# Performance work log

Hardware: AMD Instinct MI355X
Metric: run time of the kernel (lower is better)

The kernel has to match this reference:

```python
import jax, jax.numpy as jnp
import numpy as np

B, T, K, V = 64, 256, 32, 32  # batch, trace_len, net_k, vocab_len


def setup_inputs() -> dict:
    key = jax.random.key(0)
    k1, k2, k3 = jax.random.split(key, 3)
    x = jax.random.uniform(k1, (B, T, V), dtype=jnp.float32)
    w_right = jax.random.normal(k2, (K, K + 1), dtype=jnp.float32)
    w_op = jax.random.normal(k3, (K, 5 + V), dtype=jnp.float32)
    return {"x": x, "w_right": w_right, "w_op": w_op}


def _myrelu(z):
    # CenteredLayer: x<0 -> 0.01*x ; x>1 -> 0.01*x + 0.99 ; else identity
    return jnp.where(z < 0, 0.01 * z, jnp.where(z > 1, 0.01 * z + 0.99, z))


def reference(x, w_right, w_op):
    Bs, Ts, Vs = x.shape
    Ks = w_right.shape[0]
    # cal_softmax()
    sm_op = jax.nn.softmax(w_op, axis=1)
    op_w = sm_op[:, :5].T          # (5, K) operator selection weights
    atom_w = sm_op[:, 5:].T        # (V, K)
    right_w = jax.nn.softmax(w_right, axis=1)[:, :-1].T  # (K, K)

    # atom_x is loop-invariant (x and atom_w do not change across iterations)
    atom_x = jnp.einsum('btv,vk->btk', x, atom_w)  # (B, T, K)
    zcol = jnp.zeros((Bs, Ts, 1), x.dtype)   # last_x (always zeros)
    zrow = jnp.zeros((Bs, 1, Ks), x.dtype)   # end_x  (always zeros)

    def step(all_x, _):
        left = jnp.concatenate([all_x[:, :, 1:], zcol], axis=2)          # shift node dim
        right = jnp.einsum('btk,kj->btj', all_x, right_w)                # right-child mix
        nxt = all_x[:, 1:]                                               # (B, T-1, K)
        X_left = jnp.concatenate(
            [jnp.concatenate([nxt[:, :, 1:], zcol[:, 1:]], axis=2), zrow], axis=1)
        nxt_full = jnp.concatenate([nxt, zrow], axis=1)                  # (B, T, K)
        until = right + _myrelu(left + nxt_full - 1.0)
        new = _myrelu(atom_x
                      + (1.0 - left) * op_w[1]            # not
                      + X_left * op_w[3]                  # next (X)
                      + (left + right - 1.0) * op_w[2]    # and
                      + until * op_w[4])                  # until
        return new, None

    init = jnp.zeros((Bs, Ts, Ks), x.dtype)
    all_x, _ = jax.lax.scan(step, init, None, length=Ts + Ks)
    return jax.nn.sigmoid((all_x - 0.5) * 5.0)
```

## Files before the change

kernel.cpp:

```cpp
#include <hip/hip_runtime.h>
#include <math.h>

#define BB 64
#define TT 256
#define KK 32
#define VV 32
#define CH 32
#define PH 32
#define ROWS (CH + PH)
#define NPHASE ((TT + KK) / PH)
#define BPB (TT / CH)
#define NW (ROWS / 16)

#define RW_OFF    0
#define WOP_OFF   1024
#define ATOM_OFF  2240
#define STATE_OFF (ATOM_OFF + BB*TT*KK)
#define FLAG_OFF  (STATE_OFF + BB*TT*KK)

typedef __attribute__((ext_vector_type(8))) short short8;
typedef __attribute__((ext_vector_type(4))) float floatx4;

__device__ __forceinline__ float myrelu(float z) {
    return fmaf(0.01f, z, 0.99f * __builtin_amdgcn_fmed3f(z, 0.f, 1.f));
}
__device__ __forceinline__ ushort f2bf(float f) {
    union { float f; unsigned int u; } v; v.f = f;
    unsigned int r = v.u + 0x7fffu + ((v.u >> 16) & 1u);
    return (ushort)(r >> 16);
}
__device__ __forceinline__ float dpp_shl1(float v) {
    return __int_as_float(__builtin_amdgcn_update_dpp(
        0, __float_as_int(v), 0x101 , 0xF, 0xF, true));
}

__global__ void prep_kernel(const float* __restrict__ w_right,
                            const float* __restrict__ w_op,
                            float* __restrict__ ws) {
    int tid = threadIdx.x;
    float* rw  = ws + RW_OFF;
    float* wop = ws + WOP_OFF;
    if (tid < KK) {
        float v[37];
        float m = -1e30f;
        #pragma unroll
        for (int i = 0; i < 37; ++i) { v[i] = w_op[tid * 37 + i]; m = fmaxf(m, v[i]); }
        float s = 0.f;
        #pragma unroll
        for (int i = 0; i < 37; ++i) { v[i] = expf(v[i] - m); s += v[i]; }
        float inv = 1.f / s;
        #pragma unroll
        for (int i = 0; i < 37; ++i) wop[i * KK + tid] = v[i] * inv;
    } else if (tid < 2 * KK) {
        int r = tid - KK;
        float v[KK + 1];
        float m = -1e30f;
        #pragma unroll
        for (int i = 0; i <= KK; ++i) { v[i] = w_right[r * (KK + 1) + i]; m = fmaxf(m, v[i]); }
        float s = 0.f;
        #pragma unroll
        for (int i = 0; i <= KK; ++i) { v[i] = expf(v[i] - m); s += v[i]; }
        float inv = 1.f / s;
        #pragma unroll
        for (int c = 0; c < KK; ++c) rw[c * KK + r] = v[c] * inv;
    }
}

__global__ void atomx_kernel(const float* __restrict__ x, float* __restrict__ ws) {
    const float* aw = ws + WOP_OFF + 5 * KK;
    float* atom = ws + ATOM_OFF;
    int tid = threadIdx.x;
    if (blockIdx.x < 2) ((int*)(ws + FLAG_OFF))[blockIdx.x * 256 + tid] = 0;
    int k  = tid & (KK - 1);
    int bt = blockIdx.x * 8 + (tid >> 5);
    const float* xrow = x + bt * VV;
    float acc = 0.f;
    #pragma unroll
    for (int v = 0; v < VV; ++v) acc = fmaf(xrow[v], aw[v * KK + k], acc);
    atom[bt * KK + k] = acc;
}

__global__ __launch_bounds__(256, 2)
void phase_all_kernel(float* __restrict__ ws, float* __restrict__ out) {
    __shared__ float brow[2][NW + 1][36];

    const float* rw   = ws + RW_OFF;
    const float* wop  = ws + WOP_OFF;
    const float* atom = ws + ATOM_OFF;
    float*      state = ws + STATE_OFF;
    int*        flags = (int*)(ws + FLAG_OFF);

    int tid  = threadIdx.x;
    int lane = tid & 63;
    int rt   = tid >> 6;
    int lr   = lane & 15;
    int hi   = lane >> 4;
    int b  = blockIdx.x / BPB;
    int c  = blockIdx.x % BPB;
    int lo = c * CH;
    int t0 = lo + rt * 16 + lr;
    bool active = (lo + rt * 16) < TT;

    for (int i = tid; i < 2 * (NW + 1) * 36; i += 256)
        (&brow[0][0][0])[i] = 0.f;

    float* gs = state + (size_t)b * TT * KK;

    float y[8];
    #pragma unroll
    for (int q = 0; q < 8; ++q) y[q] = 0.f;

    float c0p[8], d1p[8], w3v[8], w4n[8], w4c[8];
    {
        float av[8] = {0, 0, 0, 0, 0, 0, 0, 0};
        if (active) {
            float4 a0 = *reinterpret_cast<const float4*>(&atom[((size_t)b * TT + t0) * KK + hi * 8]);
            float4 a1 = *reinterpret_cast<const float4*>(&atom[((size_t)b * TT + t0) * KK + hi * 8 + 4]);
            av[0] = a0.x; av[1] = a0.y; av[2] = a0.z; av[3] = a0.w;
            av[4] = a1.x; av[5] = a1.y; av[6] = a1.z; av[7] = a1.w;
        }
        #pragma unroll
        for (int q = 0; q < 8; ++q) {
            int j = hi * 8 + q;
            float w1 = wop[1 * KK + j];
            float w2 = wop[2 * KK + j];
            float w3 = wop[3 * KK + j];
            float w4 = wop[4 * KK + j];
            c0p[q] = av[q] + w1 - w2 - w4;
            d1p[q] = (w2 - w1) + 0.01f * w4;
            w4n[q] = 0.01f * w4;
            w4c[q] = 0.99f * w4;
            w3v[q] = w3;
        }
    }

    short8 af0, af1;
    {
        int col0 = ((lr >> 2) << 3) | (lr & 3);
        float s0 = wop[2 * KK + col0]     + wop[4 * KK + col0];
        float s1 = wop[2 * KK + col0 + 4] + wop[4 * KK + col0 + 4];
        #pragma unroll
        for (int q = 0; q < 8; ++q) {
            af0[q] = (short)f2bf(rw[(hi * 8 + q) * KK + col0] * s0);
            af1[q] = (short)f2bf(rw[(hi * 8 + q) * KK + col0 + 4] * s1);
        }
    }

    int pidx = ((lane + 16) & 63) << 2;
    __syncthreads();

    for (int p = 0; p < NPHASE; ++p) {
        for (int s = 0; s < PH; ++s) {
            int cur = s & 1;
            if (active) {
                unsigned bw0, bw1, bw2, bw3;
                asm("v_cvt_pk_bf16_f32 %0, %1, %2" : "=v"(bw0) : "v"(y[0]), "v"(y[1]));
                asm("v_cvt_pk_bf16_f32 %0, %1, %2" : "=v"(bw1) : "v"(y[2]), "v"(y[3]));
                asm("v_cvt_pk_bf16_f32 %0, %1, %2" : "=v"(bw2) : "v"(y[4]), "v"(y[5]));
                asm("v_cvt_pk_bf16_f32 %0, %1, %2" : "=v"(bw3) : "v"(y[6]), "v"(y[7]));
                union { unsigned u[4]; short8 v; } bu;
                bu.u[0] = bw0; bu.u[1] = bw1; bu.u[2] = bw2; bu.u[3] = bw3;
                floatx4 acc0 = __builtin_amdgcn_mfma_f32_16x16x32_bf16(
                    af0, bu.v, (floatx4){c0p[0], c0p[1], c0p[2], c0p[3]}, 0, 0, 0);
                floatx4 acc1 = __builtin_amdgcn_mfma_f32_16x16x32_bf16(
                    af1, bu.v, (floatx4){c0p[4], c0p[5], c0p[6], c0p[7]}, 0, 0, 0);

                float nx[8];
                #pragma unroll
                for (int q = 0; q < 8; ++q) nx[q] = dpp_shl1(y[q]);
                float lbr = __int_as_float(__builtin_amdgcn_ds_bpermute(pidx, __float_as_int(y[0])));
                float lb  = (hi == 3) ? 0.f : lbr;
                float xb  = dpp_shl1(lb);
                if (hi == 3) xb = 0.f;
                if (lr == 15) {
                    float4 n0 = *reinterpret_cast<const float4*>(&brow[cur][rt + 1][hi * 8]);
                    float4 n1 = *reinterpret_cast<const float4*>(&brow[cur][rt + 1][hi * 8 + 4]);
                    nx[0] = n0.x; nx[1] = n0.y; nx[2] = n0.z; nx[3] = n0.w;
                    nx[4] = n1.x; nx[5] = n1.y; nx[6] = n1.z; nx[7] = n1.w;
                    xb = brow[cur][rt + 1][hi * 8 + 8];
                }

                float le[8], xl[8];
                #pragma unroll
                for (int q = 0; q < 7; ++q) { le[q] = y[q + 1]; xl[q] = nx[q + 1]; }
                le[7] = lb; xl[7] = xb;

                #pragma unroll
                for (int q = 0; q < 8; ++q) {
                    float accq = (q < 4) ? acc0[q] : acc1[q - 4];
                    float sm = le[q] + nx[q];
                    float t  = __builtin_amdgcn_fmed3f(sm, 1.f, 2.f);
                    float z  = fmaf(le[q], d1p[q],
                               fmaf(nx[q], w4n[q],
                               fmaf(t, w4c[q],
                               fmaf(xl[q], w3v[q], accq))));
                    y[q] = myrelu(z);
                }
                if (lr == 0) {
                    *reinterpret_cast<float4*>(&brow[cur ^ 1][rt][hi * 8])     = make_float4(y[0], y[1], y[2], y[3]);
                    *reinterpret_cast<float4*>(&brow[cur ^ 1][rt][hi * 8 + 4]) = make_float4(y[4], y[5], y[6], y[7]);
                }
            }
            __syncthreads();
        }
        if (p == NPHASE - 1) break;

        if (rt < CH / 16 && c > 0) {
            unsigned long long* gp =
                reinterpret_cast<unsigned long long*>(gs + (size_t)t0 * KK + hi * 8);
            union { float f[8]; unsigned long long u[4]; } pk;
            #pragma unroll
            for (int q = 0; q < 8; ++q) pk.f[q] = y[q];
            #pragma unroll
            for (int w = 0; w < 4; ++w)
                __hip_atomic_store(&gp[w], pk.u[w], __ATOMIC_RELAXED, __HIP_MEMORY_SCOPE_AGENT);
        }
        __syncthreads();
        if (tid == 0) {
            if (c > 0)
                __hip_atomic_store(&flags[b * BPB + c], p + 1,
                                   __ATOMIC_RELEASE, __HIP_MEMORY_SCOPE_AGENT);
            if (c < BPB - 1) {
                while (__hip_atomic_load(&flags[b * BPB + c + 1],
                                         __ATOMIC_ACQUIRE, __HIP_MEMORY_SCOPE_AGENT) < p + 1)
                    __builtin_amdgcn_s_sleep(2);
            }
        }
        __syncthreads();
        if (active && rt >= CH / 16) {
            unsigned long long* gp =
                reinterpret_cast<unsigned long long*>(gs + (size_t)t0 * KK + hi * 8);
            union { float f[8]; unsigned long long u[4]; } pk;
            #pragma unroll
            for (int w = 0; w < 4; ++w)
                pk.u[w] = __hip_atomic_load(&gp[w], __ATOMIC_RELAXED, __HIP_MEMORY_SCOPE_AGENT);
            #pragma unroll
            for (int q = 0; q < 8; ++q) y[q] = pk.f[q];
            if (lr == 0) {
                *reinterpret_cast<float4*>(&brow[0][rt][hi * 8])     = make_float4(y[0], y[1], y[2], y[3]);
                *reinterpret_cast<float4*>(&brow[0][rt][hi * 8 + 4]) = make_float4(y[4], y[5], y[6], y[7]);
            }
        }
        __syncthreads();
    }

    if (rt < CH / 16) {
        float* op = out + ((size_t)b * TT + t0) * KK + hi * 8;
        float o[8];
        #pragma unroll
        for (int q = 0; q < 8; ++q)
            o[q] = 1.f / (1.f + __expf(-5.f * (y[q] - 0.5f)));
        *reinterpret_cast<float4*>(&op[0]) = make_float4(o[0], o[1], o[2], o[3]);
        *reinterpret_cast<float4*>(&op[4]) = make_float4(o[4], o[5], o[6], o[7]);
    }
}

extern "C" void kernel_launch(void* const* d_in, const int* in_sizes, int n_in,
                              void* d_out, int out_size, void* d_ws, size_t ws_size,
                              hipStream_t stream) {
    const float* x       = (const float*)d_in[0];
    const float* w_right = (const float*)d_in[1];
    const float* w_op    = (const float*)d_in[2];
    float* ws  = (float*)d_ws;
    float* out = (float*)d_out;

    prep_kernel<<<1, 64, 0, stream>>>(w_right, w_op, ws);
    atomx_kernel<<<BB * TT / 8, 256, 0, stream>>>(x, ws);

    void* args[] = { (void*)&ws, (void*)&out };
    hipLaunchCooperativeKernel((void*)phase_all_kernel,
                               dim3(BB * BPB), dim3(256), args, 0, stream);
}
```

Before: 225.4 us.

## Fold not/and/next/until linear terms into extra MFMA with shifted operand

Moves the per-element linear terms (left·d1, next·w4n, X_left·w3) into the MFMA A-matrices: the shifted-by-one identity terms go into af0/af1, and a second pair of MFMAs multiplies the shifted next-row state by a sparse nf matrix. This removes several FMAs and the xl/xb shuffle work from each serial step. Branches become branchless: every lane does the LDS boundary read, and the row write goes to a dummy buffer when the lane is not 0. The global state handoff switches from atomic stores to plain float4 stores plus a threadfence. The cost is doubled MFMA count on the critical path and more bf16 rounding of linear terms, which may affect accuracy.

Measured after the change: 372.6 us. 1.65x slower.

```diff
diff --git a/kernel.cpp b/kernel.cpp
--- a/kernel.cpp
+++ b/kernel.cpp
@@ -83,6 +83,7 @@
 __global__ __launch_bounds__(256, 2)
 void phase_all_kernel(float* __restrict__ ws, float* __restrict__ out) {
     __shared__ float brow[2][NW + 1][36];
+    __shared__ float dummy[64][8];
 
     const float* rw   = ws + RW_OFF;
     const float* wop  = ws + WOP_OFF;
@@ -100,6 +101,8 @@
     int lo = c * CH;
     int t0 = lo + rt * 16 + lr;
     bool active = (lo + rt * 16) < TT;
+    bool l15 = (lr == 15);
+    bool h3  = (hi == 3);
 
     for (int i = tid; i < 2 * (NW + 1) * 36; i += 256)
         (&brow[0][0][0])[i] = 0.f;
@@ -110,7 +113,7 @@
     #pragma unroll
     for (int q = 0; q < 8; ++q) y[q] = 0.f;
 
-    float c0p[8], d1p[8], w3v[8], w4n[8], w4c[8];
+    float c0p[8], w4c[8];
     {
         float av[8] = {0, 0, 0, 0, 0, 0, 0, 0};
         if (active) {
@@ -124,25 +127,34 @@
             int j = hi * 8 + q;
             float w1 = wop[1 * KK + j];
             float w2 = wop[2 * KK + j];
-            float w3 = wop[3 * KK + j];
             float w4 = wop[4 * KK + j];
             c0p[q] = av[q] + w1 - w2 - w4;
-            d1p[q] = (w2 - w1) + 0.01f * w4;
-            w4n[q] = 0.01f * w4;
             w4c[q] = 0.99f * w4;
-            w3v[q] = w3;
-        }
-    }
-
-    short8 af0, af1;
+        }
+    }
+
+    short8 af0, af1, nf0, nf1;
     {
         int col0 = ((lr >> 2) << 3) | (lr & 3);
-        float s0 = wop[2 * KK + col0]     + wop[4 * KK + col0];
-        float s1 = wop[2 * KK + col0 + 4] + wop[4 * KK + col0 + 4];
+        int col1 = col0 + 4;
+        float w1a = wop[1 * KK + col0], w2a = wop[2 * KK + col0];
+        float w3a = wop[3 * KK + col0], w4a = wop[4 * KK + col0];
+        float w1b = wop[1 * KK + col1], w2b = wop[2 * KK + col1];
+        float w3b = wop[3 * KK + col1], w4b = wop[4 * KK + col1];
+        float sa = w2a + w4a, sb = w2b + w4b;
+        float da = (w2a - w1a) + 0.01f * w4a;
+        float db = (w2b - w1b) + 0.01f * w4b;
         #pragma unroll
         for (int q = 0; q < 8; ++q) {
-            af0[q] = (short)f2bf(rw[(hi * 8 + q) * KK + col0] * s0);
-            af1[q] = (short)f2bf(rw[(hi * 8 + q) * KK + col0 + 4] * s1);
+            int k = hi * 8 + q;
+            float a0 = rw[k * KK + col0] * sa + ((k == col0 + 1) ? da : 0.f);
+            float a1 = rw[k * KK + col1] * sb + ((k == col1 + 1) ? db : 0.f);
+            af0[q] = (short)f2bf(a0);
+            af1[q] = (short)f2bf(a1);
+            float n0 = (k == col0) ? 0.01f * w4a : ((k == col0 + 1) ? w3a : 0.f);
+            float n1 = (k == col1) ? 0.01f * w4b : ((k == col1 + 1) ? w3b : 0.f);
+            nf0[q] = (short)f2bf(n0);
+            nf1[q] = (short)f2bf(n1);
         }
     }
 
@@ -153,73 +165,68 @@
         for (int s = 0; s < PH; ++s) {
             int cur = s & 1;
             if (active) {
-                unsigned bw0, bw1, bw2, bw3;
+                float nx[8];
+                #pragma unroll
+                for (int q = 0; q < 8; ++q) nx[q] = dpp_shl1(y[q]);
+                float lbr = __int_as_float(__builtin_amdgcn_ds_bpermute(pidx, __float_as_int(y[0])));
+                float4 n0 = *reinterpret_cast<const float4*>(&brow[cur][rt + 1][hi * 8]);
+                float4 n1 = *reinterpret_cast<const float4*>(&brow[cur][rt + 1][hi * 8 + 4]);
+                nx[0] = l15 ? n0.x : nx[0];  nx[1] = l15 ? n0.y : nx[1];
+                nx[2] = l15 ? n0.z : nx[2];  nx[3] = l15 ? n0.w : nx[3];
+                nx[4] = l15 ? n1.x : nx[4];  nx[5] = l15 ? n1.y : nx[5];
+                nx[6] = l15 ? n1.z : nx[6];  nx[7] = l15 ? n1.w : nx[7];
+                float lb = h3 ? 0.f : lbr;
+
+                unsigned bw0, bw1, bw2, bw3, nw0, nw1, nw2, nw3;
                 asm("v_cvt_pk_bf16_f32 %0, %1, %2" : "=v"(bw0) : "v"(y[0]), "v"(y[1]));
                 asm("v_cvt_pk_bf16_f32 %0, %1, %2" : "=v"(bw1) : "v"(y[2]), "v"(y[3]));
                 asm("v_cvt_pk_bf16_f32 %0, %1, %2" : "=v"(bw2) : "v"(y[4]), "v"(y[5]));
                 asm("v_cvt_pk_bf16_f32 %0, %1, %2" : "=v"(bw3) : "v"(y[6]), "v"(y[7]));
-                union { unsigned u[4]; short8 v; } bu;
+                asm("v_cvt_pk_bf16_f32 %0, %1, %2" : "=v"(nw0) : "v"(nx[0]), "v"(nx[1]));
+                asm("v_cvt_pk_bf16_f32 %0, %1, %2" : "=v"(nw1) : "v"(nx[2]), "v"(nx[3]));
+                asm("v_cvt_pk_bf16_f32 %0, %1, %2" : "=v"(nw2) : "v"(nx[4]), "v"(nx[5]));
+                asm("v_cvt_pk_bf16_f32 %0, %1, %2" : "=v"(nw3) : "v"(nx[6]), "v"(nx[7]));
+                union { unsigned u[4]; short8 v; } bu, nu;
                 bu.u[0] = bw0; bu.u[1] = bw1; bu.u[2] = bw2; bu.u[3] = bw3;
+                nu.u[0] = nw0; nu.u[1] = nw1; nu.u[2] = nw2; nu.u[3] = nw3;
+
                 floatx4 acc0 = __builtin_amdgcn_mfma_f32_16x16x32_bf16(
                     af0, bu.v, (floatx4){c0p[0], c0p[1], c0p[2], c0p[3]}, 0, 0, 0);
                 floatx4 acc1 = __builtin_amdgcn_mfma_f32_16x16x32_bf16(
                     af1, bu.v, (floatx4){c0p[4], c0p[5], c0p[6], c0p[7]}, 0, 0, 0);
-
-                float nx[8];
-                #pragma unroll
-                for (int q = 0; q < 8; ++q) nx[q] = dpp_shl1(y[q]);
-                float lbr = __int_as_float(__builtin_amdgcn_ds_bpermute(pidx, __float_as_int(y[0])));
-                float lb  = (hi == 3) ? 0.f : lbr;
-                float xb  = dpp_shl1(lb);
-                if (hi == 3) xb = 0.f;
-                if (lr == 15) {
-                    float4 n0 = *reinterpret_cast<const float4*>(&brow[cur][rt + 1][hi * 8]);
-                    float4 n1 = *reinterpret_cast<const float4*>(&brow[cur][rt + 1][hi * 8 + 4]);
-                    nx[0] = n0.x; nx[1] = n0.y; nx[2] = n0.z; nx[3] = n0.w;
-                    nx[4] = n1.x; nx[5] = n1.y; nx[6] = n1.z; nx[7] = n1.w;
-                    xb = brow[cur][rt + 1][hi * 8 + 8];
-                }
-
-                float le[8], xl[8];
-                #pragma unroll
-                for (int q = 0; q < 7; ++q) { le[q] = y[q + 1]; xl[q] = nx[q + 1]; }
-                le[7] = lb; xl[7] = xb;
+                acc0 = __builtin_amdgcn_mfma_f32_16x16x32_bf16(nf0, nu.v, acc0, 0, 0, 0);
+                acc1 = __builtin_amdgcn_mfma_f32_16x16x32_bf16(nf1, nu.v, acc1, 0, 0, 0);
 
                 #pragma unroll
                 for (int q = 0; q < 8; ++q) {
                     float accq = (q < 4) ? acc0[q] : acc1[q - 4];
-                    float sm = le[q] + nx[q];
+                    float le = (q < 7) ? y[q + 1] : lb;
+                    float sm = le + nx[q];
                     float t  = __builtin_amdgcn_fmed3f(sm, 1.f, 2.f);
-                    float z  = fmaf(le[q], d1p[q],
-                               fmaf(nx[q], w4n[q],
-                               fmaf(t, w4c[q],
-                               fmaf(xl[q], w3v[q], accq))));
+                    float z  = fmaf(t, w4c[q], accq);
                     y[q] = myrelu(z);
                 }
-                if (lr == 0) {
-                    *reinterpret_cast<float4*>(&brow[cur ^ 1][rt][hi * 8])     = make_float4(y[0], y[1], y[2], y[3]);
-                    *reinterpret_cast<float4*>(&brow[cur ^ 1][rt][hi * 8 + 4]) = make_float4(y[4], y[5], y[6], y[7]);
-                }
+
+                float* wp = (lr == 0) ? &brow[cur ^ 1][rt][hi * 8] : &dummy[lane][0];
+                *reinterpret_cast<float4*>(wp)     = make_float4(y[0], y[1], y[2], y[3]);
+                *reinterpret_cast<float4*>(wp + 4) = make_float4(y[4], y[5], y[6], y[7]);
             }
             __syncthreads();
         }
         if (p == NPHASE - 1) break;
 
         if (rt < CH / 16 && c > 0) {
-            unsigned long long* gp =
-                reinterpret_cast<unsigned long long*>(gs + (size_t)t0 * KK + hi * 8);
-            union { float f[8]; unsigned long long u[4]; } pk;
-            #pragma unroll
-            for (int q = 0; q < 8; ++q) pk.f[q] = y[q];
-            #pragma unroll
-            for (int w = 0; w < 4; ++w)
-                __hip_atomic_store(&gp[w], pk.u[w], __ATOMIC_RELAXED, __HIP_MEMORY_SCOPE_AGENT);
+            float* gp = gs + (size_t)t0 * KK + hi * 8;
+            *reinterpret_cast<float4*>(gp)     = make_float4(y[0], y[1], y[2], y[3]);
+            *reinterpret_cast<float4*>(gp + 4) = make_float4(y[4], y[5], y[6], y[7]);
         }
         __syncthreads();
         if (tid == 0) {
-            if (c > 0)
+            if (c > 0) {
+                __threadfence();
                 __hip_atomic_store(&flags[b * BPB + c], p + 1,
                                    __ATOMIC_RELEASE, __HIP_MEMORY_SCOPE_AGENT);
+            }
             if (c < BPB - 1) {
                 while (__hip_atomic_load(&flags[b * BPB + c + 1],
                                          __ATOMIC_ACQUIRE, __HIP_MEMORY_SCOPE_AGENT) < p + 1)
```

## Process two batch elements per block to interleave independent recurrences

Applied to the files above, without the earlier changes.

Each block now handles two batch elements (b and b+32), interleaving their MFMA and elementwise updates in one instruction stream. This halves the grid to 256 blocks and changes launch bounds to one block per SIMD target. The goal is to hide the MFMA and cross-lane latency of the serial recurrence with independent work and to halve the number of cross-block flag handshakes. The cost is more registers and more work per step in each wave.

Result: slower. 313.7 us (+39.2%).

```diff
diff --git a/kernel.cpp b/kernel.cpp
--- a/kernel.cpp
+++ b/kernel.cpp
@@ -7,10 +7,11 @@
 #define VV 32
 #define CH 32
 #define PH 32
-#define ROWS (CH + PH)
-#define NPHASE ((TT + KK) / PH)
-#define BPB (TT / CH)
-#define NW (ROWS / 16)
+#define NPHASE 9
+#define BPB 8
+#define NBP 32
+#define NW 4
+#define NTHR 256
 
 #define RW_OFF    0
 #define WOP_OFF   1024
@@ -20,6 +21,7 @@
 
 typedef __attribute__((ext_vector_type(8))) short short8;
 typedef __attribute__((ext_vector_type(4))) float floatx4;
+typedef __attribute__((ext_vector_type(4))) int intx4;
 
 __device__ __forceinline__ float myrelu(float z) {
     return fmaf(0.01f, z, 0.99f * __builtin_amdgcn_fmed3f(z, 0.f, 1.f));
@@ -29,9 +31,9 @@
     unsigned int r = v.u + 0x7fffu + ((v.u >> 16) & 1u);
     return (ushort)(r >> 16);
 }
-__device__ __forceinline__ float dpp_shl1(float v) {
+__device__ __forceinline__ float dpp_shl1_f(float v) {
     return __int_as_float(__builtin_amdgcn_update_dpp(
-        0, __float_as_int(v), 0x101 , 0xF, 0xF, true));
+        0, __float_as_int(v), 0x101, 0xF, 0xF, true));
 }
 
 __global__ void prep_kernel(const float* __restrict__ w_right,
@@ -70,7 +72,7 @@
     const float* aw = ws + WOP_OFF + 5 * KK;
     float* atom = ws + ATOM_OFF;
     int tid = threadIdx.x;
-    if (blockIdx.x < 2) ((int*)(ws + FLAG_OFF))[blockIdx.x * 256 + tid] = 0;
+    if (blockIdx.x == 0 && tid < NBP * BPB) ((int*)(ws + FLAG_OFF))[tid] = 0;
     int k  = tid & (KK - 1);
     int bt = blockIdx.x * 8 + (tid >> 5);
     const float* xrow = x + bt * VV;
@@ -80,9 +82,9 @@
     atom[bt * KK + k] = acc;
 }
 
-__global__ __launch_bounds__(256, 2)
+__global__ __launch_bounds__(NTHR, 1)
 void phase_all_kernel(float* __restrict__ ws, float* __restrict__ out) {
-    __shared__ float brow[2][NW + 1][36];
+    __shared__ float brow[2][2][NW + 1][36];
 
     const float* rw   = ws + RW_OFF;
     const float* wop  = ws + WOP_OFF;
@@ -95,57 +97,73 @@
     int rt   = tid >> 6;
     int lr   = lane & 15;
     int hi   = lane >> 4;
-    int b  = blockIdx.x / BPB;
-    int c  = blockIdx.x % BPB;
+    int bp = blockIdx.x >> 3;
+    int c  = blockIdx.x & 7;
     int lo = c * CH;
+    int bA = bp, bB = bp + NBP;
     int t0 = lo + rt * 16 + lr;
     bool active = (lo + rt * 16) < TT;
 
-    for (int i = tid; i < 2 * (NW + 1) * 36; i += 256)
-        (&brow[0][0][0])[i] = 0.f;
-
-    float* gs = state + (size_t)b * TT * KK;
-
-    float y[8];
+    for (int i = tid; i < 2 * 2 * (NW + 1) * 36; i += NTHR)
+        (&brow[0][0][0][0])[i] = 0.f;
+
+    float* gsA = state + (size_t)bA * TT * KK;
+    float* gsB = state + (size_t)bB * TT * KK;
+
+    float Ay[8], By[8];
     #pragma unroll
-    for (int q = 0; q < 8; ++q) y[q] = 0.f;
-
-    float c0p[8], d1p[8], w3v[8], w4n[8], w4c[8];
+    for (int q = 0; q < 8; ++q) { Ay[q] = 0.f; By[q] = 0.f; }
+
+    float d1p[8], w4n[8], w4c[8], w3v[8];
+    floatx4 c0Aa, c0Ab, c0Ba, c0Bb;
     {
-        float av[8] = {0, 0, 0, 0, 0, 0, 0, 0};
-        if (active) {
-            float4 a0 = *reinterpret_cast<const float4*>(&atom[((size_t)b * TT + t0) * KK + hi * 8]);
-            float4 a1 = *reinterpret_cast<const float4*>(&atom[((size_t)b * TT + t0) * KK + hi * 8 + 4]);
-            av[0] = a0.x; av[1] = a0.y; av[2] = a0.z; av[3] = a0.w;
-            av[4] = a1.x; av[5] = a1.y; av[6] = a1.z; av[7] = a1.w;
-        }
+        const float* w1p = wop + 1 * KK + hi * 8;
+        const float* w2p = wop + 2 * KK + hi * 8;
+        const float* w3p = wop + 3 * KK + hi * 8;
+        const float* w4p = wop + 4 * KK + hi * 8;
+        float avA[8], avB[8];
+        #pragma unroll
+        for (int q = 0; q < 8; ++q) { avA[q] = 0.f; avB[q] = 0.f; }
+        if (t0 < TT) {
+            float4 a0 = *reinterpret_cast<const float4*>(&atom[((size_t)bA * TT + t0) * KK + hi * 8]);
+            float4 a1 = *reinterpret_cast<const float4*>(&atom[((size_t)bA * TT + t0) * KK + hi * 8 + 4]);
+            float4 b0 = *reinterpret_cast<const float4*>(&atom[((size_t)bB * TT + t0) * KK + hi * 8]);
+            float4 b1 = *reinterpret_cast<const float4*>(&atom[((size_t)bB * TT + t0) * KK + hi * 8 + 4]);
+            avA[0] = a0.x; avA[1] = a0.y; avA[2] = a0.z; avA[3] = a0.w;
+            avA[4] = a1.x; avA[5] = a1.y; avA[6] = a1.z; avA[7] = a1.w;
+            avB[0] = b0.x; avB[1] = b0.y; avB[2] = b0.z; avB[3] = b0.w;
+            avB[4] = b1.x; avB[5] = b1.y; avB[6] = b1.z; avB[7] = b1.w;
+        }
+        float base[8];
         #pragma unroll
         for (int q = 0; q < 8; ++q) {
-            int j = hi * 8 + q;
-            float w1 = wop[1 * KK + j];
-            float w2 = wop[2 * KK + j];
-            float w3 = wop[3 * KK + j];
-            float w4 = wop[4 * KK + j];
-            c0p[q] = av[q] + w1 - w2 - w4;
-            d1p[q] = (w2 - w1) + 0.01f * w4;
-            w4n[q] = 0.01f * w4;
-            w4c[q] = 0.99f * w4;
-            w3v[q] = w3;
-        }
+            base[q] = w1p[q] - w2p[q] - w4p[q];
+            d1p[q]  = (w2p[q] - w1p[q]) + 0.01f * w4p[q];
+            w4n[q]  = 0.01f * w4p[q];
+            w4c[q]  = 0.99f * w4p[q];
+            w3v[q]  = w3p[q];
+        }
+        c0Aa = (floatx4){avA[0]+base[0], avA[1]+base[1], avA[2]+base[2], avA[3]+base[3]};
+        c0Ab = (floatx4){avA[4]+base[4], avA[5]+base[5], avA[6]+base[6], avA[7]+base[7]};
+        c0Ba = (floatx4){avB[0]+base[0], avB[1]+base[1], avB[2]+base[2], avB[3]+base[3]};
+        c0Bb = (floatx4){avB[4]+base[4], avB[5]+base[5], avB[6]+base[6], avB[7]+base[7]};
     }
 
     short8 af0, af1;
     {
         int col0 = ((lr >> 2) << 3) | (lr & 3);
-        float s0 = wop[2 * KK + col0]     + wop[4 * KK + col0];
-        float s1 = wop[2 * KK + col0 + 4] + wop[4 * KK + col0 + 4];
+        int col1 = col0 + 4;
+        float sa = wop[2 * KK + col0] + wop[4 * KK + col0];
+        float sb = wop[2 * KK + col1] + wop[4 * KK + col1];
+        int k0 = hi * 8;
         #pragma unroll
         for (int q = 0; q < 8; ++q) {
-            af0[q] = (short)f2bf(rw[(hi * 8 + q) * KK + col0] * s0);
-            af1[q] = (short)f2bf(rw[(hi * 8 + q) * KK + col0 + 4] * s1);
-        }
-    }
-
+            af0[q] = (short)f2bf(rw[(k0 + q) * KK + col0] * sa);
+            af1[q] = (short)f2bf(rw[(k0 + q) * KK + col1] * sb);
+        }
+    }
+
+    bool h3 = (hi == 3);
     int pidx = ((lane + 16) & 63) << 2;
     __syncthreads();
 
@@ -153,105 +171,152 @@
         for (int s = 0; s < PH; ++s) {
             int cur = s & 1;
             if (active) {
-                unsigned bw0, bw1, bw2, bw3;
-                asm("v_cvt_pk_bf16_f32 %0, %1, %2" : "=v"(bw0) : "v"(y[0]), "v"(y[1]));
-                asm("v_cvt_pk_bf16_f32 %0, %1, %2" : "=v"(bw1) : "v"(y[2]), "v"(y[3]));
-                asm("v_cvt_pk_bf16_f32 %0, %1, %2" : "=v"(bw2) : "v"(y[4]), "v"(y[5]));
-                asm("v_cvt_pk_bf16_f32 %0, %1, %2" : "=v"(bw3) : "v"(y[6]), "v"(y[7]));
-                union { unsigned u[4]; short8 v; } bu;
-                bu.u[0] = bw0; bu.u[1] = bw1; bu.u[2] = bw2; bu.u[3] = bw3;
-                floatx4 acc0 = __builtin_amdgcn_mfma_f32_16x16x32_bf16(
-                    af0, bu.v, (floatx4){c0p[0], c0p[1], c0p[2], c0p[3]}, 0, 0, 0);
-                floatx4 acc1 = __builtin_amdgcn_mfma_f32_16x16x32_bf16(
-                    af1, bu.v, (floatx4){c0p[4], c0p[5], c0p[6], c0p[7]}, 0, 0, 0);
-
-                float nx[8];
+                float Anx[8], Bnx[8];
                 #pragma unroll
-                for (int q = 0; q < 8; ++q) nx[q] = dpp_shl1(y[q]);
-                float lbr = __int_as_float(__builtin_amdgcn_ds_bpermute(pidx, __float_as_int(y[0])));
-                float lb  = (hi == 3) ? 0.f : lbr;
-                float xb  = dpp_shl1(lb);
-                if (hi == 3) xb = 0.f;
+                for (int q = 0; q < 8; ++q) { Anx[q] = dpp_shl1_f(Ay[q]); Bnx[q] = dpp_shl1_f(By[q]); }
+                float AlbR = __int_as_float(__builtin_amdgcn_ds_bpermute(pidx, __float_as_int(Ay[0])));
+                float BlbR = __int_as_float(__builtin_amdgcn_ds_bpermute(pidx, __float_as_int(By[0])));
+                float Alb = h3 ? 0.f : AlbR;
+                float Blb = h3 ? 0.f : BlbR;
+                float Axb = dpp_shl1_f(Alb);  if (h3) Axb = 0.f;
+                float Bxb = dpp_shl1_f(Blb);  if (h3) Bxb = 0.f;
                 if (lr == 15) {
-                    float4 n0 = *reinterpret_cast<const float4*>(&brow[cur][rt + 1][hi * 8]);
-                    float4 n1 = *reinterpret_cast<const float4*>(&brow[cur][rt + 1][hi * 8 + 4]);
-                    nx[0] = n0.x; nx[1] = n0.y; nx[2] = n0.z; nx[3] = n0.w;
-                    nx[4] = n1.x; nx[5] = n1.y; nx[6] = n1.z; nx[7] = n1.w;
-                    xb = brow[cur][rt + 1][hi * 8 + 8];
+                    const float* brA = &brow[0][cur][rt + 1][hi * 8];
+                    float4 a0 = *reinterpret_cast<const float4*>(brA);
+                    float4 a1 = *reinterpret_cast<const float4*>(brA + 4);
+                    Anx[0] = a0.x; Anx[1] = a0.y; Anx[2] = a0.z; Anx[3] = a0.w;
+                    Anx[4] = a1.x; Anx[5] = a1.y; Anx[6] = a1.z; Anx[7] = a1.w;
+                    Axb = brA[8];
+                    const float* brB = &brow[1][cur][rt + 1][hi * 8];
+                    float4 b0 = *reinterpret_cast<const float4*>(brB);
+                    float4 b1 = *reinterpret_cast<const float4*>(brB + 4);
+                    Bnx[0] = b0.x; Bnx[1] = b0.y; Bnx[2] = b0.z; Bnx[3] = b0.w;
+                    Bnx[4] = b1.x; Bnx[5] = b1.y; Bnx[6] = b1.z; Bnx[7] = b1.w;
+                    Bxb = brB[8];
                 }
 
-                float le[8], xl[8];
-                #pragma unroll
-                for (int q = 0; q < 7; ++q) { le[q] = y[q + 1]; xl[q] = nx[q + 1]; }
-                le[7] = lb; xl[7] = xb;
+                unsigned aw0, aw1, aw2, aw3, bw0, bw1, bw2, bw3;
+                asm("v_cvt_pk_bf16_f32 %0, %1, %2" : "=v"(aw0) : "v"(Ay[0]), "v"(Ay[1]));
+                asm("v_cvt_pk_bf16_f32 %0, %1, %2" : "=v"(aw1) : "v"(Ay[2]), "v"(Ay[3]));
+                asm("v_cvt_pk_bf16_f32 %0, %1, %2" : "=v"(aw2) : "v"(Ay[4]), "v"(Ay[5]));
+                asm("v_cvt_pk_bf16_f32 %0, %1, %2" : "=v"(aw3) : "v"(Ay[6]), "v"(Ay[7]));
+                short8 bvA = __builtin_bit_cast(short8,
+                    (intx4){(int)aw0, (int)aw1, (int)aw2, (int)aw3});
+                floatx4 aA0 = __builtin_amdgcn_mfma_f32_16x16x32_bf16(af0, bvA, c0Aa, 0, 0, 0);
+                floatx4 aA1 = __builtin_amdgcn_mfma_f32_16x16x32_bf16(af1, bvA, c0Ab, 0, 0, 0);
+                asm("v_cvt_pk_bf16_f32 %0, %1, %2" : "=v"(bw0) : "v"(By[0]), "v"(By[1]));
+                asm("v_cvt_pk_bf16_f32 %0, %1, %2" : "=v"(bw1) : "v"(By[2]), "v"(By[3]));
+                asm("v_cvt_pk_bf16_f32 %0, %1, %2" : "=v"(bw2) : "v"(By[4]), "v"(By[5]));
+                asm("v_cvt_pk_bf16_f32 %0, %1, %2" : "=v"(bw3) : "v"(By[6]), "v"(By[7]));
+                short8 bvB = __builtin_bit_cast(short8,
+                    (intx4){(int)bw0, (int)bw1, (int)bw2, (int)bw3});
+                floatx4 aB0 = __builtin_amdgcn_mfma_f32_16x16x32_bf16(af0, bvB, c0Ba, 0, 0, 0);
+                floatx4 aB1 = __builtin_amdgcn_mfma_f32_16x16x32_bf16(af1, bvB, c0Bb, 0, 0, 0);
 
                 #pragma unroll
                 for (int q = 0; q < 8; ++q) {
-                    float accq = (q < 4) ? acc0[q] : acc1[q - 4];
-                    float sm = le[q] + nx[q];
+                    float accq = (q < 4) ? aA0[q] : aA1[q - 4];
+                    float le = (q < 7) ? Ay[q + 1] : Alb;
+                    float xl = (q < 7) ? Anx[q + 1] : Axb;
+                    float sm = le + Anx[q];
                     float t  = __builtin_amdgcn_fmed3f(sm, 1.f, 2.f);
-                    float z  = fmaf(le[q], d1p[q],
-                               fmaf(nx[q], w4n[q],
+                    float z  = fmaf(le, d1p[q],
+                               fmaf(Anx[q], w4n[q],
                                fmaf(t, w4c[q],
-                               fmaf(xl[q], w3v[q], accq))));
-                    y[q] = myrelu(z);
+                               fmaf(xl, w3v[q], accq))));
+                    Ay[q] = myrelu(z);
                 }
+                #pragma unroll
+                for (int q = 0; q < 8; ++q) {
+                    float accq = (q < 4) ? aB0[q] : aB1[q - 4];
+                    float le = (q < 7) ? By[q + 1] : Blb;
+                    float xl = (q < 7) ? Bnx[q + 1] : Bxb;
+                    float sm = le + Bnx[q];
+                    float t  = __builtin_amdgcn_fmed3f(sm, 1.f, 2.f);
+                    float z  = fmaf(le, d1p[q],
+                               fmaf(Bnx[q], w4n[q],
+                               fmaf(t, w4c[q],
+                               fmaf(xl, w3v[q], accq))));
+                    By[q] = myrelu(z);
+                }
+
                 if (lr == 0) {
-                    *reinterpret_cast<float4*>(&brow[cur ^ 1][rt][hi * 8])     = make_float4(y[0], y[1], y[2], y[3]);
-                    *reinterpret_cast<float4*>(&brow[cur ^ 1][rt][hi * 8 + 4]) = make_float4(y[4], y[5], y[6], y[7]);
+                    float* wA = &brow[0][cur ^ 1][rt][hi * 8];
+                    *reinterpret_cast<float4*>(wA)     = make_float4(Ay[0], Ay[1], Ay[2], Ay[3]);
+                    *reinterpret_cast<float4*>(wA + 4) = make_float4(Ay[4], Ay[5], Ay[6], Ay[7]);
+                    float* wB = &brow[1][cur ^ 1][rt][hi * 8];
+                    *reinterpret_cast<float4*>(wB)     = make_float4(By[0], By[1], By[2], By[3]);
+                    *reinterpret_cast<float4*>(wB + 4) = make_float4(By[4], By[5], By[6], By[7]);
                 }
             }
             __syncthreads();
         }
         if (p == NPHASE - 1) break;
 
-        if (rt < CH / 16 && c > 0) {
-            unsigned long long* gp =
-                reinterpret_cast<unsigned long long*>(gs + (size_t)t0 * KK + hi * 8);
-            union { float f[8]; unsigned long long u[4]; } pk;
-            #pragma unroll
-            for (int q = 0; q < 8; ++q) pk.f[q] = y[q];
-            #pragma unroll
-            for (int w = 0; w < 4; ++w)
-                __hip_atomic_store(&gp[w], pk.u[w], __ATOMIC_RELAXED, __HIP_MEMORY_SCOPE_AGENT);
+        if (rt < 2 && c > 0) {
+            float* gA = gsA + (size_t)t0 * KK + hi * 8;
+            *reinterpret_cast<float4*>(gA)     = make_float4(Ay[0], Ay[1], Ay[2], Ay[3]);
+            *reinterpret_cast<float4*>(gA + 4) = make_float4(Ay[4], Ay[5], Ay[6], Ay[7]);
+            float* gB = gsB + (size_t)t0 * KK + hi * 8;
+            *reinterpret_cast<float4*>(gB)     = make_float4(By[0], By[1], By[2], By[3]);
+            *reinterpret_cast<float4*>(gB + 4) = make_float4(By[4], By[5], By[6], By[7]);
         }
         __syncthreads();
         if (tid == 0) {
             if (c > 0)
-                __hip_atomic_store(&flags[b * BPB + c], p + 1,
+                __hip_atomic_store(&flags[bp * BPB + c], p + 1,
                                    __ATOMIC_RELEASE, __HIP_MEMORY_SCOPE_AGENT);
             if (c < BPB - 1) {
-                while (__hip_atomic_load(&flags[b * BPB + c + 1],
+                while (__hip_atomic_load(&flags[bp * BPB + c + 1],
                                          __ATOMIC_ACQUIRE, __HIP_MEMORY_SCOPE_AGENT) < p + 1)
                     __builtin_amdgcn_s_sleep(2);
             }
         }
         __syncthreads();
-        if (active && rt >= CH / 16) {
-            unsigned long long* gp =
-                reinterpret_cast<unsigned long long*>(gs + (size_t)t0 * KK + hi * 8);
-            union { float f[8]; unsigned long long u[4]; } pk;
-            #pragma unroll
-            for (int w = 0; w < 4; ++w)
-                pk.u[w] = __hip_atomic_load(&gp[w], __ATOMIC_RELAXED, __HIP_MEMORY_SCOPE_AGENT);
-            #pragma unroll
-            for (int q = 0; q < 8; ++q) y[q] = pk.f[q];
+        if (active && rt >= 2) {
+            unsigned long long* gA = reinterpret_cast<unsigned long long*>(gsA + (size_t)t0 * KK + hi * 8);
+            unsigned long long* gB = reinterpret_cast<unsigned long long*>(gsB + (size_t)t0 * KK + hi * 8);
+            unsigned long long a0 = __hip_atomic_load(&gA[0], __ATOMIC_RELAXED, __HIP_MEMORY_SCOPE_AGENT);
+            unsigned long long a1 = __hip_atomic_load(&gA[1], __ATOMIC_RELAXED, __HIP_MEMORY_SCOPE_AGENT);
+            unsigned long long a2 = __hip_atomic_load(&gA[2], __ATOMIC_RELAXED, __HIP_MEMORY_SCOPE_AGENT);
+            unsigned long long a3 = __hip_atomic_load(&gA[3], __ATOMIC_RELAXED, __HIP_MEMORY_SCOPE_AGENT);
+            unsigned long long b0 = __hip_atomic_load(&gB[0], __ATOMIC_RELAXED, __HIP_MEMORY_SCOPE_AGENT);
+            unsigned long long b1 = __hip_atomic_load(&gB[1], __ATOMIC_RELAXED, __HIP_MEMORY_SCOPE_AGENT);
+            unsigned long long b2 = __hip_atomic_load(&gB[2], __ATOMIC_RELAXED, __HIP_MEMORY_SCOPE_AGENT);
+            unsigned long long b3 = __hip_atomic_load(&gB[3], __ATOMIC_RELAXED, __HIP_MEMORY_SCOPE_AGENT);
+            Ay[0] = __uint_as_float((unsigned)a0); Ay[1] = __uint_as_float((unsigned)(a0 >> 32));
+            Ay[2] = __uint_as_float((unsigned)a1); Ay[3] = __uint_as_float((unsigned)(a1 >> 32));
+            Ay[4] = __uint_as_float((unsigned)a2); Ay[5] = __uint_as_float((unsigned)(a2 >> 32));
+            Ay[6] = __uint_as_float((unsigned)a3); Ay[7] = __uint_as_float((unsigned)(a3 >> 32));
+            By[0] = __uint_as_float((unsigned)b0); By[1] = __uint_as_float((unsigned)(b0 >> 32));
+            By[2] = __uint_as_float((unsigned)b1); By[3] = __uint_as_float((unsigned)(b1 >> 32));
+            By[4] = __uint_as_float((unsigned)b2); By[5] = __uint_as_float((unsigned)(b2 >> 32));
+            By[6] = __uint_as_float((unsigned)b3); By[7] = __uint_as_float((unsigned)(b3 >> 32));
             if (lr == 0) {
-                *reinterpret_cast<float4*>(&brow[0][rt][hi * 8])     = make_float4(y[0], y[1], y[2], y[3]);
-                *reinterpret_cast<float4*>(&brow[0][rt][hi * 8 + 4]) = make_float4(y[4], y[5], y[6], y[7]);
+                float* wA = &brow[0][0][rt][hi * 8];
+                *reinterpret_cast<float4*>(wA)     = make_float4(Ay[0], Ay[1], Ay[2], Ay[3]);
+                *reinterpret_cast<float4*>(wA + 4) = make_float4(Ay[4], Ay[5], Ay[6], Ay[7]);
+                float* wB = &brow[1][0][rt][hi * 8];
+                *reinterpret_cast<float4*>(wB)     = make_float4(By[0], By[1], By[2], By[3]);
+                *reinterpret_cast<float4*>(wB + 4) = make_float4(By[4], By[5], By[6], By[7]);
             }
         }
         __syncthreads();
     }
 
-    if (rt < CH / 16) {
-        float* op = out + ((size_t)b * TT + t0) * KK + hi * 8;
-        float o[8];
-        #pragma unroll
-        for (int q = 0; q < 8; ++q)
-            o[q] = 1.f / (1.f + __expf(-5.f * (y[q] - 0.5f)));
-        *reinterpret_cast<float4*>(&op[0]) = make_float4(o[0], o[1], o[2], o[3]);
-        *reinterpret_cast<float4*>(&op[4]) = make_float4(o[4], o[5], o[6], o[7]);
+    if (rt < 2) {
+        float* oA = out + ((size_t)bA * TT + t0) * KK + hi * 8;
+        float* oB = out + ((size_t)bB * TT + t0) * KK + hi * 8;
+        float oa[8], ob[8];
+        #pragma unroll
+        for (int q = 0; q < 8; ++q) {
+            oa[q] = 1.f / (1.f + __expf(-5.f * (Ay[q] - 0.5f)));
+            ob[q] = 1.f / (1.f + __expf(-5.f * (By[q] - 0.5f)));
+        }
+        *reinterpret_cast<float4*>(&oA[0]) = make_float4(oa[0], oa[1], oa[2], oa[3]);
+        *reinterpret_cast<float4*>(&oA[4]) = make_float4(oa[4], oa[5], oa[6], oa[7]);
+        *reinterpret_cast<float4*>(&oB[0]) = make_float4(ob[0], ob[1], ob[2], ob[3]);
+        *reinterpret_cast<float4*>(&oB[4]) = make_float4(ob[4], ob[5], ob[6], ob[7]);
     }
 }
 
@@ -269,5 +334,5 @@
 
     void* args[] = { (void*)&ws, (void*)&out };
     hipLaunchCooperativeKernel((void*)phase_all_kernel,
-                               dim3(BB * BPB), dim3(256), args, 0, stream);
-}
+                               dim3(NBP * BPB), dim3(NTHR), args, 0, stream);
+}
```
